# Optimization experiments

Hardware: AMD Instinct MI355X
Metric: run time of the kernel (lower is better)

Reference implementation:

```python
import jax, jax.numpy as jnp
import numpy as np

B, SQ, SK, H, NH = 4, 512, 2048, 1024, 16
HD = H // NH
LN_EPS = 1e-12
NEG_INF = float('-inf')


def setup_inputs() -> dict:
    key = jax.random.key(0)
    ks = jax.random.split(key, 6)
    hidden_states = jax.random.normal(ks[0], (B, SQ, H), dtype=jnp.float32)
    encoder_hidden_states = jax.random.normal(ks[1], (B, SK, H), dtype=jnp.float32)
    mask = jax.random.randint(ks[2], (B, SK), 0, 2).astype(jnp.int32)
    mask = mask.at[:, 0].set(1)  # guarantee >=1 valid key per row (avoid all -inf softmax)
    scale = 1.0 / np.sqrt(H)
    q_w = jax.random.normal(ks[3], (H, H), dtype=jnp.float32) * scale
    k_w = jax.random.normal(ks[4], (H, H), dtype=jnp.float32) * scale
    return {
        'hidden_states': hidden_states,
        'encoder_hidden_states': encoder_hidden_states,
        'encoder_attention_mask': mask,
        'q_w': q_w,
        'q_b': jnp.zeros((H,), jnp.float32),
        'k_w': k_w,
        'k_b': jnp.zeros((H,), jnp.float32),
        'ln_g': jnp.ones((H,), jnp.float32),
        'ln_b': jnp.zeros((H,), jnp.float32),
    }


def _layernorm(x, g, b):
    mu = jnp.mean(x, axis=-1, keepdims=True)
    var = jnp.mean(jnp.square(x - mu), axis=-1, keepdims=True)
    return (x - mu) * jax.lax.rsqrt(var + LN_EPS) * g + b


def reference(hidden_states, encoder_hidden_states, encoder_attention_mask,
              q_w, q_b, k_w, k_b, ln_g, ln_b):
    bsz, sq, _ = hidden_states.shape
    hs = _layernorm(hidden_states, ln_g, ln_b)
    # torch Linear: y = x @ W.T + b
    q = (hs @ q_w.T + q_b).reshape(bsz, sq, NH, HD).transpose(0, 2, 1, 3)      # b h q d
    k = (encoder_hidden_states @ k_w.T + k_b).reshape(bsz, -1, NH, HD).transpose(0, 2, 1, 3)  # b h k d
    v = encoder_hidden_states.reshape(bsz, -1, NH, HD).transpose(0, 2, 1, 3)   # b h k d (no v projection)
    scores = jnp.einsum('bhqd,bhkd->bhqk', q, k) / np.sqrt(HD)
    scores = jnp.where(encoder_attention_mask[:, None, None, :] == 0, NEG_INF, scores)
    probs = jax.nn.softmax(scores, axis=-1)
    ctx = jnp.einsum('bhqk,bhkd->bhqd', probs, v)
    ctx = ctx.transpose(0, 2, 1, 3).reshape(bsz, sq, H)
    return ctx, scores
```

## Files before the change

### kernel.cpp

```cpp
#include <hip/hip_runtime.h>
#include <math.h>

#define H 1024
#define NH 16
#define HD 64
#define B_ 4
#define SQ 512
#define SK 2048
#define MASKED_SCORE -1e30f

typedef unsigned short ushort_t;
typedef __attribute__((ext_vector_type(8))) short short8_t;
typedef __attribute__((ext_vector_type(4))) float f32x4;
typedef __attribute__((ext_vector_type(4))) unsigned short us4;

__device__ inline ushort_t bf_hi(float x) { return (ushort_t)(__float_as_uint(x) >> 16); }
__device__ inline ushort_t bf_lo(float x) {
    float hf = __uint_as_float(__float_as_uint(x) & 0xffff0000u);
    return (ushort_t)(__float_as_uint(x - hf) >> 16);
}

__global__ __launch_bounds__(256) void ln_split_kernel(const float* __restrict__ x,
                                                       const float* __restrict__ g,
                                                       const float* __restrict__ bb,
                                                       ushort_t* __restrict__ hi,
                                                       ushort_t* __restrict__ lo) {
    const int row = blockIdx.x;
    const int tid = threadIdx.x;
    const float4 v = *(const float4*)&x[(size_t)row * H + tid * 4];
    float s  = v.x + v.y + v.z + v.w;
    float ss = v.x * v.x + v.y * v.y + v.z * v.z + v.w * v.w;
    #pragma unroll
    for (int o = 32; o > 0; o >>= 1) { s += __shfl_down(s, o); ss += __shfl_down(ss, o); }
    __shared__ float red_s[4], red_ss[4];
    const int wv = tid >> 6, ln = tid & 63;
    if (ln == 0) { red_s[wv] = s; red_ss[wv] = ss; }
    __syncthreads();
    s  = red_s[0] + red_s[1] + red_s[2] + red_s[3];
    ss = red_ss[0] + red_ss[1] + red_ss[2] + red_ss[3];
    const float mu   = s * (1.0f / H);
    const float var  = ss * (1.0f / H) - mu * mu;
    const float rstd = rsqrtf(var + 1e-12f);
    const float4 gv = *(const float4*)&g[tid * 4];
    const float4 bv = *(const float4*)&bb[tid * 4];
    float o0 = (v.x - mu) * rstd * gv.x + bv.x;
    float o1 = (v.y - mu) * rstd * gv.y + bv.y;
    float o2 = (v.z - mu) * rstd * gv.z + bv.z;
    float o3 = (v.w - mu) * rstd * gv.w + bv.w;
    us4 h4, l4;
    h4.x = bf_hi(o0); h4.y = bf_hi(o1); h4.z = bf_hi(o2); h4.w = bf_hi(o3);
    l4.x = bf_lo(o0); l4.y = bf_lo(o1); l4.z = bf_lo(o2); l4.w = bf_lo(o3);
    *(us4*)&hi[(size_t)row * H + tid * 4] = h4;
    *(us4*)&lo[(size_t)row * H + tid * 4] = l4;
}

__global__ __launch_bounds__(256) void ehs_split_tr(const float* __restrict__ ehs,
                                                    ushort_t* __restrict__ eh, ushort_t* __restrict__ el,
                                                    ushort_t* __restrict__ vh, ushort_t* __restrict__ vl) {
    __shared__ float Tf[64][68];
    const int tid = threadIdx.x;
    const int k0 = blockIdx.x * 64;
    const int h = blockIdx.y, b = blockIdx.z;
    const int r = tid >> 2, c0 = (tid & 3) << 4;
    const size_t gidx = (size_t)(b * SK + k0 + r) * H + h * HD + c0;
    float fv[16];
    #pragma unroll
    for (int j = 0; j < 4; ++j) {
        const float4 v = *(const float4*)&ehs[gidx + 4 * j];
        fv[4 * j + 0] = v.x; fv[4 * j + 1] = v.y; fv[4 * j + 2] = v.z; fv[4 * j + 3] = v.w;
        Tf[r][c0 + 4 * j + 0] = v.x; Tf[r][c0 + 4 * j + 1] = v.y;
        Tf[r][c0 + 4 * j + 2] = v.z; Tf[r][c0 + 4 * j + 3] = v.w;
    }
    short8_t H0, H1, L0, L1;
    #pragma unroll
    for (int j = 0; j < 8; ++j) {
        H0[j] = (short)bf_hi(fv[j]);     H1[j] = (short)bf_hi(fv[8 + j]);
        L0[j] = (short)bf_lo(fv[j]);     L1[j] = (short)bf_lo(fv[8 + j]);
    }
    *(short8_t*)&eh[gidx] = H0; *(short8_t*)&eh[gidx + 8] = H1;
    *(short8_t*)&el[gidx] = L0; *(short8_t*)&el[gidx + 8] = L1;
    __syncthreads();
    const int d = tid >> 2, kb = (tid & 3) << 4;
    float tv[16];
    #pragma unroll
    for (int i = 0; i < 16; ++i) tv[i] = Tf[kb + i][d];
    short8_t Vh0, Vh1, Vl0, Vl1;
    #pragma unroll
    for (int j = 0; j < 8; ++j) {
        Vh0[j] = (short)bf_hi(tv[j]);     Vh1[j] = (short)bf_hi(tv[8 + j]);
        Vl0[j] = (short)bf_lo(tv[j]);     Vl1[j] = (short)bf_lo(tv[8 + j]);
    }
    const size_t vg = ((size_t)((b * NH + h) * HD + d)) * SK + k0 + kb;
    *(short8_t*)&vh[vg] = Vh0; *(short8_t*)&vh[vg + 8] = Vh1;
    *(short8_t*)&vl[vg] = Vl0; *(short8_t*)&vl[vg + 8] = Vl1;
}

__global__ __launch_bounds__(256) void split_kernel(const float* __restrict__ src,
                                                    ushort_t* __restrict__ hi,
                                                    ushort_t* __restrict__ lo, int n4) {
    const int i = blockIdx.x * 256 + threadIdx.x;
    if (i >= n4) return;
    const float4 v = ((const float4*)src)[i];
    us4 h4, l4;
    h4.x = bf_hi(v.x); h4.y = bf_hi(v.y); h4.z = bf_hi(v.z); h4.w = bf_hi(v.w);
    l4.x = bf_lo(v.x); l4.y = bf_lo(v.y); l4.z = bf_lo(v.z); l4.w = bf_lo(v.w);
    ((us4*)hi)[i] = h4;
    ((us4*)lo)[i] = l4;
}

__global__ __launch_bounds__(256, 2) void gemm_planes(
        const ushort_t* __restrict__ Ah_g, const ushort_t* __restrict__ Al_g,
        const ushort_t* __restrict__ Wh_g, const ushort_t* __restrict__ Wl_g,
        const float* __restrict__ bias,
        ushort_t* __restrict__ Chi, ushort_t* __restrict__ Clo) {
    __shared__ ushort_t Ah[128 * 64], Al[128 * 64], Wh[128 * 64], Wl[128 * 64];
    const int tid = threadIdx.x;
    const int cpx = gridDim.x >> 3;
    const int L = (blockIdx.x & 7) * cpx + (blockIdx.x >> 3);
    const int m0 = (L >> 3) * 128, n0 = (L & 7) * 128;
    const int lane = tid & 63, wid = tid >> 6;
    const int wr = wid >> 1, wc = wid & 1;
    const int fr = lane & 15, fs = lane >> 4;

    int srow[4], sch[4], lidx[4];
    #pragma unroll
    for (int i = 0; i < 4; ++i) {
        const int c = i * 256 + tid;
        srow[i] = c >> 3; sch[i] = c & 7;
        lidx[i] = srow[i] * 64 + ((sch[i] ^ (srow[i] & 7)) << 3);
    }

    short8_t rAh[4], rAl[4], rWh[4], rWl[4];
    auto gload = [&](int k0) {
        #pragma unroll
        for (int i = 0; i < 4; ++i) {
            const size_t ga = (size_t)(m0 + srow[i]) * H + k0 + (sch[i] << 3);
            const size_t gw = (size_t)(n0 + srow[i]) * H + k0 + (sch[i] << 3);
            rAh[i] = *(const short8_t*)&Ah_g[ga];
            rAl[i] = *(const short8_t*)&Al_g[ga];
            rWh[i] = *(const short8_t*)&Wh_g[gw];
            rWl[i] = *(const short8_t*)&Wl_g[gw];
        }
    };

    f32x4 acc[4][4];
    #pragma unroll
    for (int i = 0; i < 4; ++i)
        #pragma unroll
        for (int j = 0; j < 4; ++j) acc[i][j] = (f32x4)0.f;

    gload(0);
    for (int kt = 0; kt < 16; ++kt) {
        #pragma unroll
        for (int i = 0; i < 4; ++i) {
            *(short8_t*)&Ah[lidx[i]] = rAh[i];
            *(short8_t*)&Al[lidx[i]] = rAl[i];
            *(short8_t*)&Wh[lidx[i]] = rWh[i];
            *(short8_t*)&Wl[lidx[i]] = rWl[i];
        }
        __syncthreads();
        if (kt < 15) gload((kt + 1) * 64);
        #pragma unroll
        for (int ks = 0; ks < 2; ++ks) {
            short8_t ah[4], al[4], bh[4], bl[4];
            #pragma unroll
            for (int mi = 0; mi < 4; ++mi) {
                const int rr = wr * 64 + mi * 16 + fr;
                const int idx = rr * 64 + ((((ks << 2) + fs) ^ (rr & 7)) << 3);
                ah[mi] = *(const short8_t*)&Ah[idx];
                al[mi] = *(const short8_t*)&Al[idx];
            }
            #pragma unroll
            for (int ni = 0; ni < 4; ++ni) {
                const int rr = wc * 64 + ni * 16 + fr;
                const int idx = rr * 64 + ((((ks << 2) + fs) ^ (rr & 7)) << 3);
                bh[ni] = *(const short8_t*)&Wh[idx];
                bl[ni] = *(const short8_t*)&Wl[idx];
            }
            #pragma unroll
            for (int mi = 0; mi < 4; ++mi)
                #pragma unroll
                for (int ni = 0; ni < 4; ++ni) {
                    acc[mi][ni] = __builtin_amdgcn_mfma_f32_16x16x32_bf16(ah[mi], bh[ni], acc[mi][ni], 0, 0, 0);
                    acc[mi][ni] = __builtin_amdgcn_mfma_f32_16x16x32_bf16(ah[mi], bl[ni], acc[mi][ni], 0, 0, 0);
                    acc[mi][ni] = __builtin_amdgcn_mfma_f32_16x16x32_bf16(al[mi], bh[ni], acc[mi][ni], 0, 0, 0);
                }
        }
        __syncthreads();
    }
    #pragma unroll
    for (int ni = 0; ni < 4; ++ni) {
        const int col = n0 + wc * 64 + ni * 16 + fr;
        const float bv = bias[col];
        #pragma unroll
        for (int mi = 0; mi < 4; ++mi) {
            const int row = m0 + wr * 64 + mi * 16 + (fs << 2);
            #pragma unroll
            for (int r2 = 0; r2 < 4; ++r2) {
                const float v = acc[mi][ni][r2] + bv;
                Chi[(size_t)(row + r2) * H + col] = bf_hi(v);
                Clo[(size_t)(row + r2) * H + col] = bf_lo(v);
            }
        }
    }
}

__global__ __launch_bounds__(256, 2) void attn_mfma(
        const ushort_t* __restrict__ Qh_g, const ushort_t* __restrict__ Ql_g,
        const ushort_t* __restrict__ Kh_g, const ushort_t* __restrict__ Kl_g,
        const ushort_t* __restrict__ Vh_g, const ushort_t* __restrict__ Vl_g,
        const int* __restrict__ mask,
        float* __restrict__ ctx_out, float* __restrict__ sc_out) {
    __shared__ ushort_t Qh[64 * 64], Ql[64 * 64];
    __shared__ ushort_t Kh[64 * 64], Kl[64 * 64];
    __shared__ ushort_t Vh[64 * 64], Vl[64 * 64];
    __shared__ ushort_t Ph[64 * 72], Pl[64 * 72];
    __shared__ int Ms[64];
    const int tid = threadIdx.x, lane = tid & 63, w = tid >> 6;
    const int fr = lane & 15, fs = lane >> 4;
    const int L = (blockIdx.x & 7) * 64 + (blockIdx.x >> 3);
    const int b = L >> 7, h = (L >> 3) & 15, q0 = (L & 7) * 64;

    int srow[2], sch[2], lidx[2];
    #pragma unroll
    for (int i = 0; i < 2; ++i) {
        const int c = i * 256 + tid;
        srow[i] = c >> 3; sch[i] = c & 7;
        lidx[i] = srow[i] * 64 + ((sch[i] ^ (srow[i] & 7)) << 3);
    }

    short8_t rk[8];
    auto kvload = [&](int k0) {
        #pragma unroll
        for (int i = 0; i < 2; ++i) {
            const size_t gk = (size_t)(b * SK + k0 + srow[i]) * H + h * HD + (sch[i] << 3);
            const size_t gv = ((size_t)((b * NH + h) * HD + srow[i])) * SK + k0 + (sch[i] << 3);
            rk[0 + i] = *(const short8_t*)&Kh_g[gk];
            rk[2 + i] = *(const short8_t*)&Kl_g[gk];
            rk[4 + i] = *(const short8_t*)&Vh_g[gv];
            rk[6 + i] = *(const short8_t*)&Vl_g[gv];
        }
    };
    auto kvwrite = [&]() {
        #pragma unroll
        for (int i = 0; i < 2; ++i) {
            *(short8_t*)&Kh[lidx[i]] = rk[0 + i];
            *(short8_t*)&Kl[lidx[i]] = rk[2 + i];
            *(short8_t*)&Vh[lidx[i]] = rk[4 + i];
            *(short8_t*)&Vl[lidx[i]] = rk[6 + i];
        }
    };

    {
        short8_t rq[4];
        #pragma unroll
        for (int i = 0; i < 2; ++i) {
            const size_t gq = (size_t)(b * SQ + q0 + srow[i]) * H + h * HD + (sch[i] << 3);
            rq[i]     = *(const short8_t*)&Qh_g[gq];
            rq[2 + i] = *(const short8_t*)&Ql_g[gq];
        }
        kvload(0);
        #pragma unroll
        for (int i = 0; i < 2; ++i) {
            *(short8_t*)&Qh[lidx[i]] = rq[i];
            *(short8_t*)&Ql[lidx[i]] = rq[2 + i];
        }
        kvwrite();
        if (tid < 64) Ms[tid] = mask[b * SK + tid];
    }
    __syncthreads();

    short8_t qh[2], ql[2];
    #pragma unroll
    for (int ks = 0; ks < 2; ++ks) {
        const int rr = w * 16 + fr;
        const int idx = rr * 64 + ((((ks << 2) + fs) ^ (rr & 7)) << 3);
        qh[ks] = *(const short8_t*)&Qh[idx];
        ql[ks] = *(const short8_t*)&Ql[idx];
    }

    f32x4 cacc[4];
    #pragma unroll
    for (int ni = 0; ni < 4; ++ni) cacc[ni] = (f32x4)0.f;
    float m_r[4] = {-INFINITY, -INFINITY, -INFINITY, -INFINITY};
    float l_r[4] = {0.f, 0.f, 0.f, 0.f};

    int mreg = 0;
    for (int kc = 0; kc < 32; ++kc) {
        const int k0 = kc * 64;
        if (kc < 31) {
            kvload(k0 + 64);
            if (tid < 64) mreg = mask[b * SK + k0 + 64 + tid];
        }
        f32x4 sacc[4];
        #pragma unroll
        for (int ni = 0; ni < 4; ++ni) sacc[ni] = (f32x4)0.f;
        #pragma unroll
        for (int ks = 0; ks < 2; ++ks) {
            short8_t kbh[4], kbl[4];
            #pragma unroll
            for (int ni = 0; ni < 4; ++ni) {
                const int rr = ni * 16 + fr;
                const int idx = rr * 64 + ((((ks << 2) + fs) ^ (rr & 7)) << 3);
                kbh[ni] = *(const short8_t*)&Kh[idx];
                kbl[ni] = *(const short8_t*)&Kl[idx];
            }
            #pragma unroll
            for (int ni = 0; ni < 4; ++ni) {
                sacc[ni] = __builtin_amdgcn_mfma_f32_16x16x32_bf16(qh[ks], kbh[ni], sacc[ni], 0, 0, 0);
                sacc[ni] = __builtin_amdgcn_mfma_f32_16x16x32_bf16(qh[ks], kbl[ni], sacc[ni], 0, 0, 0);
                sacc[ni] = __builtin_amdgcn_mfma_f32_16x16x32_bf16(ql[ks], kbh[ni], sacc[ni], 0, 0, 0);
            }
        }
        int mv[4];
        #pragma unroll
        for (int ni = 0; ni < 4; ++ni) mv[ni] = Ms[ni * 16 + fr];

        const size_t scbase = ((size_t)((b * NH + h) * SQ + q0 + w * 16 + (fs << 2))) * SK + k0;
        #pragma unroll
        for (int r2 = 0; r2 < 4; ++r2) {
            float sv[4];
            #pragma unroll
            for (int ni = 0; ni < 4; ++ni) sv[ni] = sacc[ni][r2] * 0.125f;
            #pragma unroll
            for (int ni = 0; ni < 4; ++ni)
                sc_out[scbase + (size_t)r2 * SK + ni * 16 + fr] = mv[ni] ? sv[ni] : MASKED_SCORE;
            float x0 = mv[0] ? sv[0] : -INFINITY;
            float x1 = mv[1] ? sv[1] : -INFINITY;
            float x2 = mv[2] ? sv[2] : -INFINITY;
            float x3 = mv[3] ? sv[3] : -INFINITY;
            float cm = fmaxf(fmaxf(x0, x1), fmaxf(x2, x3));
            cm = fmaxf(cm, __shfl_xor(cm, 1));
            cm = fmaxf(cm, __shfl_xor(cm, 2));
            cm = fmaxf(cm, __shfl_xor(cm, 4));
            cm = fmaxf(cm, __shfl_xor(cm, 8));
            const float mn = fmaxf(m_r[r2], cm);
            const float scf = (m_r[r2] == mn) ? 1.0f : __expf(m_r[r2] - mn);
            float p[4], ps = 0.f;
            #pragma unroll
            for (int ni = 0; ni < 4; ++ni) {
                p[ni] = mv[ni] ? __expf(sv[ni] - mn) : 0.f;
                ps += p[ni];
            }
            ps += __shfl_xor(ps, 1);
            ps += __shfl_xor(ps, 2);
            ps += __shfl_xor(ps, 4);
            ps += __shfl_xor(ps, 8);
            l_r[r2] = l_r[r2] * scf + ps;
            m_r[r2] = mn;
            #pragma unroll
            for (int ni = 0; ni < 4; ++ni) cacc[ni][r2] *= scf;
            const int prow = w * 16 + (fs << 2) + r2;
            #pragma unroll
            for (int ni = 0; ni < 4; ++ni) {
                Ph[prow * 72 + ni * 16 + fr] = bf_hi(p[ni]);
                Pl[prow * 72 + ni * 16 + fr] = bf_lo(p[ni]);
            }
        }
        #pragma unroll
        for (int ks = 0; ks < 2; ++ks) {
            const int pidx = (w * 16 + fr) * 72 + ks * 32 + (fs << 3);
            const short8_t pah = *(const short8_t*)&Ph[pidx];
            const short8_t pal = *(const short8_t*)&Pl[pidx];
            #pragma unroll
            for (int ni = 0; ni < 4; ++ni) {
                const int rr = ni * 16 + fr;
                const int idx = rr * 64 + ((((ks << 2) + fs) ^ (rr & 7)) << 3);
                const short8_t vbh = *(const short8_t*)&Vh[idx];
                const short8_t vbl = *(const short8_t*)&Vl[idx];
                cacc[ni] = __builtin_amdgcn_mfma_f32_16x16x32_bf16(pah, vbh, cacc[ni], 0, 0, 0);
                cacc[ni] = __builtin_amdgcn_mfma_f32_16x16x32_bf16(pah, vbl, cacc[ni], 0, 0, 0);
                cacc[ni] = __builtin_amdgcn_mfma_f32_16x16x32_bf16(pal, vbh, cacc[ni], 0, 0, 0);
            }
        }
        __syncthreads();
        if (kc < 31) {
            kvwrite();
            if (tid < 64) Ms[tid] = mreg;
        }
        __syncthreads();
    }
    #pragma unroll
    for (int ni = 0; ni < 4; ++ni)
        #pragma unroll
        for (int r2 = 0; r2 < 4; ++r2) {
            const float v = cacc[ni][r2] / l_r[r2];
            ctx_out[(size_t)(b * SQ + q0 + w * 16 + (fs << 2) + r2) * H + h * HD + ni * 16 + fr] = v;
        }
}

extern "C" void kernel_launch(void* const* d_in, const int* in_sizes, int n_in,
                              void* d_out, int out_size, void* d_ws, size_t ws_size,
                              hipStream_t stream) {
    const float* hs_in = (const float*)d_in[0];
    const float* ehs   = (const float*)d_in[1];
    const int*   msk   = (const int*)d_in[2];
    const float* q_w   = (const float*)d_in[3];
    const float* q_b   = (const float*)d_in[4];
    const float* k_w   = (const float*)d_in[5];
    const float* k_b   = (const float*)d_in[6];
    const float* ln_g  = (const float*)d_in[7];
    const float* ln_b  = (const float*)d_in[8];

    float* ctx = (float*)d_out;
    float* sc  = ctx + (size_t)B_ * SQ * H;

    ushort_t* wsu = (ushort_t*)d_ws;
    ushort_t* Vth = wsu;
    ushort_t* Vtl = Vth + (size_t)8 * 1024 * 1024;
    ushort_t* Khp = Vtl + (size_t)8 * 1024 * 1024;
    ushort_t* Klp = Khp + (size_t)8 * 1024 * 1024;
    ushort_t* Qhp = Klp + (size_t)8 * 1024 * 1024;
    ushort_t* Qlp = Qhp + (size_t)2 * 1024 * 1024;

    ushort_t* scr = (ushort_t*)sc;
    ushort_t* Ehp = scr;
    ushort_t* Elp = Ehp + (size_t)8 * 1024 * 1024;
    ushort_t* HSh = Elp + (size_t)8 * 1024 * 1024;
    ushort_t* HSl = HSh + (size_t)2 * 1024 * 1024;
    ushort_t* QWh = HSl + (size_t)2 * 1024 * 1024;
    ushort_t* QWl = QWh + (size_t)1024 * 1024;
    ushort_t* KWh = QWl + (size_t)1024 * 1024;
    ushort_t* KWl = KWh + (size_t)1024 * 1024;

    ln_split_kernel<<<B_ * SQ, 256, 0, stream>>>(hs_in, ln_g, ln_b, HSh, HSl);
    ehs_split_tr<<<dim3(SK / 64, NH, B_), 256, 0, stream>>>(ehs, Ehp, Elp, Vth, Vtl);
    split_kernel<<<1024, 256, 0, stream>>>(q_w, QWh, QWl, (H * H) / 4);
    split_kernel<<<1024, 256, 0, stream>>>(k_w, KWh, KWl, (H * H) / 4);
    gemm_planes<<<(B_ * SQ / 128) * (H / 128), 256, 0, stream>>>(HSh, HSl, QWh, QWl, q_b, Qhp, Qlp);
    gemm_planes<<<(B_ * SK / 128) * (H / 128), 256, 0, stream>>>(Ehp, Elp, KWh, KWl, k_b, Khp, Klp);
    attn_mfma<<<512, 256, 0, stream>>>(Qhp, Qlp, Khp, Klp, Vth, Vtl, msk, ctx, sc);
}
```

Baseline: 502.7 us.

## Merge weight splits and Q/K GEMMs, stage score tiles through LDS for coalesced stores

The two weight-split launches become one kernel, and the Q and K projection GEMMs become a single 640-block launch. This removes launches and the tail of the smaller GEMM. In attention, score tiles are staged in the now-free Q shared buffer (swizzled) and written out as float4 rows, replacing scattered scalar stores to the large scores output. The online softmax now rescales only when the running max increases, at the cost of a branch and an extra barrier.

```diff
diff --git a/kernel.cpp b/kernel.cpp
--- a/kernel.cpp
+++ b/kernel.cpp
@@ -95,11 +95,15 @@
     *(short8_t*)&vl[vg] = Vl0; *(short8_t*)&vl[vg + 8] = Vl1;
 }
 
-__global__ __launch_bounds__(256) void split_kernel(const float* __restrict__ src,
-                                                    ushort_t* __restrict__ hi,
-                                                    ushort_t* __restrict__ lo, int n4) {
-    const int i = blockIdx.x * 256 + threadIdx.x;
-    if (i >= n4) return;
+__global__ __launch_bounds__(256) void split2_kernel(const float* __restrict__ s0,
+                                                     const float* __restrict__ s1,
+                                                     ushort_t* __restrict__ h0, ushort_t* __restrict__ l0,
+                                                     ushort_t* __restrict__ h1, ushort_t* __restrict__ l1,
+                                                     int n4) {
+    int i = blockIdx.x * 256 + threadIdx.x;
+    const float* src; ushort_t* hi; ushort_t* lo;
+    if (i < n4) { src = s0; hi = h0; lo = l0; }
+    else        { src = s1; hi = h1; lo = l1; i -= n4; }
     const float4 v = ((const float4*)src)[i];
     us4 h4, l4;
     h4.x = bf_hi(v.x); h4.y = bf_hi(v.y); h4.z = bf_hi(v.z); h4.w = bf_hi(v.w);
@@ -108,16 +112,27 @@
     ((us4*)lo)[i] = l4;
 }
 
-__global__ __launch_bounds__(256, 2) void gemm_planes(
-        const ushort_t* __restrict__ Ah_g, const ushort_t* __restrict__ Al_g,
-        const ushort_t* __restrict__ Wh_g, const ushort_t* __restrict__ Wl_g,
-        const float* __restrict__ bias,
-        ushort_t* __restrict__ Chi, ushort_t* __restrict__ Clo) {
+__global__ __launch_bounds__(256, 2) void gemm_dual(
+        const ushort_t* __restrict__ QAh, const ushort_t* __restrict__ QAl,
+        const ushort_t* __restrict__ QWh_g, const ushort_t* __restrict__ QWl_g,
+        const float* __restrict__ q_bias, ushort_t* __restrict__ QCh, ushort_t* __restrict__ QCl,
+        const ushort_t* __restrict__ KAh, const ushort_t* __restrict__ KAl,
+        const ushort_t* __restrict__ KWh_g, const ushort_t* __restrict__ KWl_g,
+        const float* __restrict__ k_bias, ushort_t* __restrict__ KCh, ushort_t* __restrict__ KCl) {
     __shared__ ushort_t Ah[128 * 64], Al[128 * 64], Wh[128 * 64], Wl[128 * 64];
     const int tid = threadIdx.x;
     const int cpx = gridDim.x >> 3;
-    const int L = (blockIdx.x & 7) * cpx + (blockIdx.x >> 3);
-    const int m0 = (L >> 3) * 128, n0 = (L & 7) * 128;
+    const int L = ((int)blockIdx.x & 7) * cpx + ((int)blockIdx.x >> 3);
+    const bool isQ = L < 128;
+    const int Li = isQ ? L : L - 128;
+    const ushort_t* Ah_g = isQ ? QAh : KAh;
+    const ushort_t* Al_g = isQ ? QAl : KAl;
+    const ushort_t* Wh_g = isQ ? QWh_g : KWh_g;
+    const ushort_t* Wl_g = isQ ? QWl_g : KWl_g;
+    const float*    bias = isQ ? q_bias : k_bias;
+    ushort_t* Chi = isQ ? QCh : KCh;
+    ushort_t* Clo = isQ ? QCl : KCl;
+    const int m0 = (Li >> 3) * 128, n0 = (Li & 7) * 128;
     const int lane = tid & 63, wid = tid >> 6;
     const int wr = wid >> 1, wc = wid & 1;
     const int fr = lane & 15, fs = lane >> 4;
@@ -205,20 +220,22 @@
     }
 }
 
+#define SIDX(q, c) ((q) * 64 + ((((c)) ^ ((q) & 15)) << 2))
 __global__ __launch_bounds__(256, 2) void attn_mfma(
         const ushort_t* __restrict__ Qh_g, const ushort_t* __restrict__ Ql_g,
         const ushort_t* __restrict__ Kh_g, const ushort_t* __restrict__ Kl_g,
         const ushort_t* __restrict__ Vh_g, const ushort_t* __restrict__ Vl_g,
         const int* __restrict__ mask,
         float* __restrict__ ctx_out, float* __restrict__ sc_out) {
-    __shared__ ushort_t Qh[64 * 64], Ql[64 * 64];
+    __shared__ ushort_t QS[2 * 64 * 64];
     __shared__ ushort_t Kh[64 * 64], Kl[64 * 64];
     __shared__ ushort_t Vh[64 * 64], Vl[64 * 64];
     __shared__ ushort_t Ph[64 * 72], Pl[64 * 72];
     __shared__ int Ms[64];
+    float* Sbuf = (float*)QS;
     const int tid = threadIdx.x, lane = tid & 63, w = tid >> 6;
     const int fr = lane & 15, fs = lane >> 4;
-    const int L = (blockIdx.x & 7) * 64 + (blockIdx.x >> 3);
+    const int L = ((int)blockIdx.x & 7) * 64 + ((int)blockIdx.x >> 3);
     const int b = L >> 7, h = (L >> 3) & 15, q0 = (L & 7) * 64;
 
     int srow[2], sch[2], lidx[2];
@@ -262,8 +279,8 @@
         kvload(0);
         #pragma unroll
         for (int i = 0; i < 2; ++i) {
-            *(short8_t*)&Qh[lidx[i]] = rq[i];
-            *(short8_t*)&Ql[lidx[i]] = rq[2 + i];
+            *(short8_t*)&QS[lidx[i]]        = rq[i];
+            *(short8_t*)&QS[4096 + lidx[i]] = rq[2 + i];
         }
         kvwrite();
         if (tid < 64) Ms[tid] = mask[b * SK + tid];
@@ -275,15 +292,19 @@
     for (int ks = 0; ks < 2; ++ks) {
         const int rr = w * 16 + fr;
         const int idx = rr * 64 + ((((ks << 2) + fs) ^ (rr & 7)) << 3);
-        qh[ks] = *(const short8_t*)&Qh[idx];
-        ql[ks] = *(const short8_t*)&Ql[idx];
-    }
+        qh[ks] = *(const short8_t*)&QS[idx];
+        ql[ks] = *(const short8_t*)&QS[4096 + idx];
+    }
+    __syncthreads();
 
     f32x4 cacc[4];
     #pragma unroll
     for (int ni = 0; ni < 4; ++ni) cacc[ni] = (f32x4)0.f;
     float m_r[4] = {-INFINITY, -INFINITY, -INFINITY, -INFINITY};
     float l_r[4] = {0.f, 0.f, 0.f, 0.f};
+
+    const int oq = tid >> 2, oc0 = (tid & 3) << 2;
+    const size_t sobase = ((size_t)((b * NH + h) * SQ + q0 + oq)) * SK;
 
     int mreg = 0;
     for (int kc = 0; kc < 32; ++kc) {
@@ -316,15 +337,17 @@
         #pragma unroll
         for (int ni = 0; ni < 4; ++ni) mv[ni] = Ms[ni * 16 + fr];
 
-        const size_t scbase = ((size_t)((b * NH + h) * SQ + q0 + w * 16 + (fs << 2))) * SK + k0;
         #pragma unroll
         for (int r2 = 0; r2 < 4; ++r2) {
+            const int q = w * 16 + (fs << 2) + r2;
             float sv[4];
             #pragma unroll
             for (int ni = 0; ni < 4; ++ni) sv[ni] = sacc[ni][r2] * 0.125f;
             #pragma unroll
-            for (int ni = 0; ni < 4; ++ni)
-                sc_out[scbase + (size_t)r2 * SK + ni * 16 + fr] = mv[ni] ? sv[ni] : MASKED_SCORE;
+            for (int ni = 0; ni < 4; ++ni) {
+                const int c = (ni << 2) + (fr >> 2);
+                Sbuf[SIDX(q, c) + (fr & 3)] = mv[ni] ? sv[ni] : MASKED_SCORE;
+            }
             float x0 = mv[0] ? sv[0] : -INFINITY;
             float x1 = mv[1] ? sv[1] : -INFINITY;
             float x2 = mv[2] ? sv[2] : -INFINITY;
@@ -334,27 +357,29 @@
             cm = fmaxf(cm, __shfl_xor(cm, 2));
             cm = fmaxf(cm, __shfl_xor(cm, 4));
             cm = fmaxf(cm, __shfl_xor(cm, 8));
-            const float mn = fmaxf(m_r[r2], cm);
-            const float scf = (m_r[r2] == mn) ? 1.0f : __expf(m_r[r2] - mn);
+            if (cm > m_r[r2]) {
+                const float mn = cm;
+                const float scf = (m_r[r2] == -INFINITY) ? 0.f : __expf(m_r[r2] - mn);
+                l_r[r2] *= scf;
+                #pragma unroll
+                for (int ni = 0; ni < 4; ++ni) cacc[ni][r2] *= scf;
+                m_r[r2] = mn;
+            }
             float p[4], ps = 0.f;
             #pragma unroll
             for (int ni = 0; ni < 4; ++ni) {
-                p[ni] = mv[ni] ? __expf(sv[ni] - mn) : 0.f;
+                p[ni] = mv[ni] ? __expf(sv[ni] - m_r[r2]) : 0.f;
                 ps += p[ni];
             }
             ps += __shfl_xor(ps, 1);
             ps += __shfl_xor(ps, 2);
             ps += __shfl_xor(ps, 4);
             ps += __shfl_xor(ps, 8);
-            l_r[r2] = l_r[r2] * scf + ps;
-            m_r[r2] = mn;
-            #pragma unroll
-            for (int ni = 0; ni < 4; ++ni) cacc[ni][r2] *= scf;
-            const int prow = w * 16 + (fs << 2) + r2;
-            #pragma unroll
-            for (int ni = 0; ni < 4; ++ni) {
-                Ph[prow * 72 + ni * 16 + fr] = bf_hi(p[ni]);
-                Pl[prow * 72 + ni * 16 + fr] = bf_lo(p[ni]);
+            l_r[r2] += ps;
+            #pragma unroll
+            for (int ni = 0; ni < 4; ++ni) {
+                Ph[q * 72 + ni * 16 + fr] = bf_hi(p[ni]);
+                Pl[q * 72 + ni * 16 + fr] = bf_lo(p[ni]);
             }
         }
         #pragma unroll
@@ -374,6 +399,12 @@
             }
         }
         __syncthreads();
+        #pragma unroll
+        for (int j = 0; j < 4; ++j) {
+            const int c = oc0 + j;
+            const float4 v4 = *(const float4*)&Sbuf[SIDX(oq, c)];
+            *(float4*)&sc_out[sobase + k0 + (c << 2)] = v4;
+        }
         if (kc < 31) {
             kvwrite();
             if (tid < 64) Ms[tid] = mreg;
@@ -425,9 +456,8 @@
 
     ln_split_kernel<<<B_ * SQ, 256, 0, stream>>>(hs_in, ln_g, ln_b, HSh, HSl);
     ehs_split_tr<<<dim3(SK / 64, NH, B_), 256, 0, stream>>>(ehs, Ehp, Elp, Vth, Vtl);
-    split_kernel<<<1024, 256, 0, stream>>>(q_w, QWh, QWl, (H * H) / 4);
-    split_kernel<<<1024, 256, 0, stream>>>(k_w, KWh, KWl, (H * H) / 4);
-    gemm_planes<<<(B_ * SQ / 128) * (H / 128), 256, 0, stream>>>(HSh, HSl, QWh, QWl, q_b, Qhp, Qlp);
-    gemm_planes<<<(B_ * SK / 128) * (H / 128), 256, 0, stream>>>(Ehp, Elp, KWh, KWl, k_b, Khp, Klp);
+    split2_kernel<<<2048, 256, 0, stream>>>(q_w, k_w, QWh, QWl, KWh, KWl, (H * H) / 4);
+    gemm_dual<<<640, 256, 0, stream>>>(HSh, HSl, QWh, QWl, q_b, Qhp, Qlp,
+                                       Ehp, Elp, KWh, KWl, k_b, Khp, Klp);
     attn_mfma<<<512, 256, 0, stream>>>(Qhp, Qlp, Khp, Klp, Vth, Vtl, msk, ctx, sc);
 }
```

After: 510.5 us. Within noise of the previous version (+1.6%).
